# Performance work log

Measured on AMD Instinct MI355X. Metric: run time of the kernel, lower is better.

## Reference

```python
import jax, jax.numpy as jnp
import numpy as np

B, F, L, D = 256, 4, 64, 768
HID = (F + F) * 200  # 1600
NEG = -1e10


def setup_inputs() -> dict:
    key = jax.random.key(0)
    ks = jax.random.split(key, 8)
    left = jax.random.normal(ks[0], (B, F, L, D), dtype=jnp.float32)
    right = jax.random.normal(ks[1], (B, F, L, D), dtype=jnp.float32)
    # emulate ragged padding: last quarter of tokens are zero (masked out)
    left = left.at[:, :, 3 * L // 4 :, :].set(0.0)
    right = right.at[:, :, 3 * L // 4 :, :].set(0.0)
    femb_l = jax.random.normal(ks[2], (F, D), dtype=jnp.float32)
    femb_r = jax.random.normal(ks[3], (F, D), dtype=jnp.float32)
    empty_attr = jax.random.normal(ks[4], (D,), dtype=jnp.float32) * 0.05
    in_dim = 2 * F * D
    W1 = jax.random.normal(ks[5], (HID, in_dim), dtype=jnp.float32) * (1.0 / np.sqrt(in_dim))
    b1 = jnp.zeros((HID,), dtype=jnp.float32)
    W2 = jax.random.normal(ks[6], (2, HID), dtype=jnp.float32) * (1.0 / np.sqrt(HID))
    b2 = jnp.full((2,), -np.log((1 - 0.01) / 0.01), dtype=jnp.float32)
    return {"left": left, "right": right, "femb_l": femb_l, "femb_r": femb_r,
            "empty_attr": empty_attr, "W1": W1, "b1": b1, "W2": W2, "b2": b2}


def _attribute_matching(v, femb, empty_attr):
    # v: [B, F, L, D], femb: [F, D]
    tok_mask = (v != 0).sum(axis=-1) > 0          # [B, F, L]
    attr_mask = tok_mask.any(axis=-1)              # [B, F]
    logits = jnp.einsum('bfld,fd->bfl', v, femb)   # per-field attention scores
    logits = logits + jnp.where(tok_mask, 0.0, NEG)
    w = jax.nn.softmax(logits, axis=2)             # masked softmax over tokens
    summary = jnp.einsum('bfl,bfld->bfd', w, v)    # attention pooling
    return jnp.where(attr_mask[..., None], summary, empty_attr)  # [B, F, D]


def reference(left, right, femb_l, femb_r, empty_attr, W1, b1, W2, b2):
    l_rep = _attribute_matching(left, femb_l, empty_attr)
    r_rep = _attribute_matching(right, femb_r, empty_attr)
    concat = jnp.concatenate([l_rep, r_rep], axis=1).reshape(left.shape[0], -1)
    h = jax.nn.relu(concat @ W1.T + b1)
    return h @ W2.T + b2  # [B, 2]
```

## Files before the change

kernel.cpp:

```cpp
#include <hip/hip_runtime.h>

typedef __attribute__((ext_vector_type(8))) short short8;
typedef __attribute__((ext_vector_type(4))) short short4_t;
typedef __attribute__((ext_vector_type(4))) float f32x4;

#define NEGBIG -1e10f

__device__ __forceinline__ unsigned short f2bf(float x) {
  unsigned int u = __float_as_uint(x);
  u += 0x7FFFu + ((u >> 16) & 1u);
  return (unsigned short)(u >> 16);
}
__device__ __forceinline__ unsigned pack2(float a, float b) {
  unsigned ua = __float_as_uint(a), ub = __float_as_uint(b);
  ua += 0x7FFFu + ((ua >> 16) & 1u);
  ub += 0x7FFFu + ((ub >> 16) & 1u);
  return (ua >> 16) | (ub & 0xFFFF0000u);
}
__device__ __forceinline__ float lo_bf(unsigned p) { return __uint_as_float(p << 16); }
__device__ __forceinline__ float hi_bf(unsigned p) { return __uint_as_float(p & 0xFFFF0000u); }

__device__ __forceinline__ float4 mul4(float4 a, float s) {
  float4 r; r.x = a.x*s; r.y = a.y*s; r.z = a.z*s; r.w = a.w*s; return r;
}
__device__ __forceinline__ float4 add4(float4 a, float4 b) {
  float4 r; r.x = a.x+b.x; r.y = a.y+b.y; r.z = a.z+b.z; r.w = a.w+b.w; return r;
}

__global__ __launch_bounds__(512, 3) void pool_kernel(
    const float* __restrict__ left, const float* __restrict__ right,
    const float* __restrict__ femb_l, const float* __restrict__ femb_r,
    const float* __restrict__ empty_attr,
    unsigned short* __restrict__ concat)
{
  int bid  = blockIdx.x;
  int side = bid >> 10;
  int rem  = bid & 1023;
  int f    = rem & 3;
  int b    = rem >> 2;
  const float* v    = (side ? right : left) + (size_t)rem * 64 * 768;
  const float* femb = (side ? femb_r : femb_l) + f * 768;

  int tid = threadIdx.x, wave = tid >> 6, lane = tid & 63;

  const float4* fp = (const float4*)femb;
  float4 f0 = fp[lane], f1 = fp[lane + 64], f2 = fp[lane + 128];

  const float4* vp = (const float4*)(v + (size_t)wave * 8 * 768);

  float d[8];
  unsigned pk0[8], pk1[8], pk2[8], pk3[8], pk4[8], pk5[8];
  unsigned nzmask = 0;

  #pragma unroll
  for (int t = 0; t < 8; ++t) {
    float4 x0 = vp[t * 192 + lane];
    float4 x1 = vp[t * 192 + 64 + lane];
    float4 x2 = vp[t * 192 + 128 + lane];
    d[t] = x0.x*f0.x + x0.y*f0.y + x0.z*f0.z + x0.w*f0.w
         + x1.x*f1.x + x1.y*f1.y + x1.z*f1.z + x1.w*f1.w
         + x2.x*f2.x + x2.y*f2.y + x2.z*f2.z + x2.w*f2.w;
    unsigned nzb = __float_as_uint(x0.x) | __float_as_uint(x0.y)
                 | __float_as_uint(x0.z) | __float_as_uint(x0.w)
                 | __float_as_uint(x1.x) | __float_as_uint(x1.y)
                 | __float_as_uint(x1.z) | __float_as_uint(x1.w)
                 | __float_as_uint(x2.x) | __float_as_uint(x2.y)
                 | __float_as_uint(x2.z) | __float_as_uint(x2.w);
    nzmask |= (nzb != 0u) ? (1u << t) : 0u;
    pk0[t] = pack2(x0.x, x0.y); pk1[t] = pack2(x0.z, x0.w);
    pk2[t] = pack2(x1.x, x1.y); pk3[t] = pack2(x1.z, x1.w);
    pk4[t] = pack2(x2.x, x2.y); pk5[t] = pack2(x2.z, x2.w);
  }

  #pragma unroll
  for (int sh = 32; sh > 0; sh >>= 1) {
    d[0] += __shfl_xor(d[0], sh);
    d[1] += __shfl_xor(d[1], sh);
    d[2] += __shfl_xor(d[2], sh);
    d[3] += __shfl_xor(d[3], sh);
    d[4] += __shfl_xor(d[4], sh);
    d[5] += __shfl_xor(d[5], sh);
    d[6] += __shfl_xor(d[6], sh);
    d[7] += __shfl_xor(d[7], sh);
    nzmask |= __shfl_xor(nzmask, sh);
  }

  float l[8], e[8];
  #pragma unroll
  for (int t = 0; t < 8; ++t)
    l[t] = d[t] + (((nzmask >> t) & 1u) ? 0.f : NEGBIG);
  float m01 = fmaxf(l[0], l[1]), m23 = fmaxf(l[2], l[3]);
  float m45 = fmaxf(l[4], l[5]), m67 = fmaxf(l[6], l[7]);
  float m_w = fmaxf(fmaxf(m01, m23), fmaxf(m45, m67));
  #pragma unroll
  for (int t = 0; t < 8; ++t) e[t] = __expf(l[t] - m_w);
  float s_w = ((e[0]+e[1]) + (e[2]+e[3])) + ((e[4]+e[5]) + (e[6]+e[7]));

  __shared__ float m_lds[8], s_lds[8];
  __shared__ int   nz_lds[8];
  __shared__ float acc_lds[8 * 768];

  if (lane == 0) { m_lds[wave] = m_w; s_lds[wave] = s_w; nz_lds[wave] = (nzmask != 0u); }

  float4 A0 = {0,0,0,0}, A1 = {0,0,0,0}, A2 = {0,0,0,0};
  #pragma unroll
  for (int t = 0; t < 8; ++t) {
    float c = e[t];
    A0.x += c * lo_bf(pk0[t]); A0.y += c * hi_bf(pk0[t]);
    A0.z += c * lo_bf(pk1[t]); A0.w += c * hi_bf(pk1[t]);
    A1.x += c * lo_bf(pk2[t]); A1.y += c * hi_bf(pk2[t]);
    A1.z += c * lo_bf(pk3[t]); A1.w += c * hi_bf(pk3[t]);
    A2.x += c * lo_bf(pk4[t]); A2.y += c * hi_bf(pk4[t]);
    A2.z += c * lo_bf(pk5[t]); A2.w += c * hi_bf(pk5[t]);
  }

  __syncthreads();
  float M = m_lds[0];
  #pragma unroll
  for (int w = 1; w < 8; ++w) M = fmaxf(M, m_lds[w]);
  float S = 0.f;
  #pragma unroll
  for (int w = 0; w < 8; ++w) S += s_lds[w] * __expf(m_lds[w] - M);
  float scale = __expf(m_w - M) / S;

  float4* al = (float4*)acc_lds;
  al[wave * 192 +       lane] = mul4(A0, scale);
  al[wave * 192 +  64 + lane] = mul4(A1, scale);
  al[wave * 192 + 128 + lane] = mul4(A2, scale);
  __syncthreads();

  if (tid < 192) {
    float4 A = add4(add4(add4(al[tid], al[192 + tid]),
                         add4(al[384 + tid], al[576 + tid])),
                    add4(add4(al[768 + tid], al[960 + tid]),
                         add4(al[1152 + tid], al[1344 + tid])));
    int has = nz_lds[0] | nz_lds[1] | nz_lds[2] | nz_lds[3]
            | nz_lds[4] | nz_lds[5] | nz_lds[6] | nz_lds[7];
    float4 r;
    if (has) r = A;
    else     r = ((const float4*)empty_attr)[tid];
    ushort4 o;
    o.x = f2bf(r.x); o.y = f2bf(r.y); o.z = f2bf(r.z); o.w = f2bf(r.w);
    size_t base = ((size_t)b * 8 + side * 4 + f) * 192;
    ((ushort4*)concat)[base + tid] = o;
  }
}

__global__ __launch_bounds__(256) void gemm1_kernel(
    const unsigned short* __restrict__ A,
    const float* __restrict__ W1,
    float* __restrict__ Hpart)
{
  const int K = 6144, N = 1600, KC = 768;
  int colb = blockIdx.x;
  int kc   = blockIdx.y;
  int col0 = colb * 16;
  int tid = threadIdx.x, wave = tid >> 6, lane = tid & 63;

  __shared__ short wlds[96 * 16 * 8];

  const float* wsrc = W1 + (size_t)col0 * K + kc * KC;
  #pragma unroll
  for (int i = 0; i < 12; ++i) {
    int flat4 = tid + 256 * i;
    int col = flat4 / 192;
    int k   = (flat4 % 192) * 4;
    float4 w = *(const float4*)(wsrc + (size_t)col * K + k);
    short4_t o;
    o[0] = (short)f2bf(w.x); o[1] = (short)f2bf(w.y);
    o[2] = (short)f2bf(w.z); o[3] = (short)f2bf(w.w);
    *(short4_t*)(wlds + (k >> 3) * 128 + col * 8 + (k & 7)) = o;
  }
  __syncthreads();

  int lr = lane & 15;
  const short* a0 = (const short*)A + (size_t)(wave * 64 + lr) * K + kc * KC + (lane >> 4) * 8;
  const short* bptr = wlds + (lane >> 4) * 128 + lr * 8;

  f32x4 acc0 = {}, acc1 = {}, acc2 = {}, acc3 = {};

  #pragma unroll 4
  for (int ks = 0; ks < 24; ++ks) {
    short8 bf  = *(const short8*)(bptr + ks * 512);
    short8 af0 = *(const short8*)(a0 + ks * 32);
    short8 af1 = *(const short8*)(a0 + ks * 32 + 16 * K);
    short8 af2 = *(const short8*)(a0 + ks * 32 + 32 * K);
    short8 af3 = *(const short8*)(a0 + ks * 32 + 48 * K);
    acc0 = __builtin_amdgcn_mfma_f32_16x16x32_bf16(af0, bf, acc0, 0, 0, 0);
    acc1 = __builtin_amdgcn_mfma_f32_16x16x32_bf16(af1, bf, acc1, 0, 0, 0);
    acc2 = __builtin_amdgcn_mfma_f32_16x16x32_bf16(af2, bf, acc2, 0, 0, 0);
    acc3 = __builtin_amdgcn_mfma_f32_16x16x32_bf16(af3, bf, acc3, 0, 0, 0);
  }

  int ccol = lane & 15;
  int crow = (lane >> 4) * 4;
  float* hp = Hpart + (size_t)kc * 256 * N + (size_t)col0 + ccol;
  f32x4 accs[4] = {acc0, acc1, acc2, acc3};
  #pragma unroll
  for (int i = 0; i < 4; ++i) {
    int r = wave * 64 + i * 16 + crow;
    #pragma unroll
    for (int q = 0; q < 4; ++q)
      hp[(size_t)(r + q) * N] = accs[i][q];
  }
}

__global__ __launch_bounds__(256) void epilogue_kernel(
    const float* __restrict__ Hpart, const float* __restrict__ b1,
    const float* __restrict__ W2, const float* __restrict__ b2,
    float* __restrict__ out)
{
  const int N = 1600;
  int b = blockIdx.x, tid = threadIdx.x;
  int wave = tid >> 6, lane = tid & 63;
  float s0 = 0.f, s1 = 0.f;
  for (int c = tid; c < N; c += 256) {
    float acc = 0.f;
    #pragma unroll
    for (int kc = 0; kc < 8; ++kc)
      acc += Hpart[((size_t)kc * 256 + b) * N + c];
    float h = fmaxf(acc + b1[c], 0.f);
    s0 += h * W2[c];
    s1 += h * W2[N + c];
  }
  #pragma unroll
  for (int s = 32; s > 0; s >>= 1) {
    s0 += __shfl_xor(s0, s);
    s1 += __shfl_xor(s1, s);
  }
  __shared__ float r0[4], r1[4];
  if (lane == 0) { r0[wave] = s0; r1[wave] = s1; }
  __syncthreads();
  if (tid == 0) {
    out[b * 2 + 0] = r0[0] + r0[1] + r0[2] + r0[3] + b2[0];
    out[b * 2 + 1] = r1[0] + r1[1] + r1[2] + r1[3] + b2[1];
  }
}

extern "C" void kernel_launch(void* const* d_in, const int* in_sizes, int n_in,
                              void* d_out, int out_size, void* d_ws, size_t ws_size,
                              hipStream_t stream) {
  const float* left       = (const float*)d_in[0];
  const float* right      = (const float*)d_in[1];
  const float* femb_l     = (const float*)d_in[2];
  const float* femb_r     = (const float*)d_in[3];
  const float* empty_attr = (const float*)d_in[4];
  const float* W1         = (const float*)d_in[5];
  const float* b1         = (const float*)d_in[6];
  const float* W2         = (const float*)d_in[7];
  const float* b2         = (const float*)d_in[8];
  float* out = (float*)d_out;

  char* ws = (char*)d_ws;
  unsigned short* concat = (unsigned short*)ws;
  float*          Hpart  = (float*)(ws + 3145728);

  hipLaunchKernelGGL(pool_kernel, dim3(2048), dim3(512), 0, stream,
                     left, right, femb_l, femb_r, empty_attr, concat);
  hipLaunchKernelGGL(gemm1_kernel, dim3(100, 8), dim3(256), 0, stream,
                     concat, W1, Hpart);
  hipLaunchKernelGGL(epilogue_kernel, dim3(256), dim3(256), 0, stream,
                     Hpart, b1, W2, b2, out);
}
```

Before: 144.3 us.

## Split pooling into half-panel partial blocks plus a merge kernel

The single pooling kernel, which used one 512-thread block per (side,b,f) panel, is split into a partial kernel: 4096 blocks of 256 threads, each handling 32 tokens and writing an unnormalized partial sum plus (max, sum, has) metadata. A new merge kernel then combines the two halves with a log-sum-exp rescale, applies the empty-attribute fallback and writes the bf16 concat. The goal is smaller blocks and finer-grained scheduling with higher occupancy for the bandwidth-bound read of the inputs. The cost is an extra kernel launch and a write and re-read of 12 MB of fp32 partials, stored in the Hpart workspace.

```diff
diff --git a/kernel.cpp b/kernel.cpp
--- a/kernel.cpp
+++ b/kernel.cpp
@@ -27,18 +27,19 @@
   float4 r; r.x = a.x+b.x; r.y = a.y+b.y; r.z = a.z+b.z; r.w = a.w+b.w; return r;
 }
 
-__global__ __launch_bounds__(512, 3) void pool_kernel(
+__global__ __launch_bounds__(256) void pool_partial(
     const float* __restrict__ left, const float* __restrict__ right,
     const float* __restrict__ femb_l, const float* __restrict__ femb_r,
-    const float* __restrict__ empty_attr,
-    unsigned short* __restrict__ concat)
-{
-  int bid  = blockIdx.x;
-  int side = bid >> 10;
-  int rem  = bid & 1023;
-  int f    = rem & 3;
-  int b    = rem >> 2;
-  const float* v    = (side ? right : left) + (size_t)rem * 64 * 768;
+    float* __restrict__ partials,
+    float4* __restrict__ meta)
+{
+  int bid   = blockIdx.x;
+  int panel = bid >> 1;
+  int half  = bid & 1;
+  int side  = panel >> 10;
+  int rem   = panel & 1023;
+  int f     = rem & 3;
+  const float* v    = (side ? right : left) + (size_t)rem * 64 * 768 + (size_t)half * 32 * 768;
   const float* femb = (side ? femb_r : femb_l) + f * 768;
 
   int tid = threadIdx.x, wave = tid >> 6, lane = tid & 63;
@@ -96,9 +97,9 @@
   for (int t = 0; t < 8; ++t) e[t] = __expf(l[t] - m_w);
   float s_w = ((e[0]+e[1]) + (e[2]+e[3])) + ((e[4]+e[5]) + (e[6]+e[7]));
 
-  __shared__ float m_lds[8], s_lds[8];
-  __shared__ int   nz_lds[8];
-  __shared__ float acc_lds[8 * 768];
+  __shared__ float m_lds[4], s_lds[4];
+  __shared__ int   nz_lds[4];
+  __shared__ float acc_lds[4 * 768];
 
   if (lane == 0) { m_lds[wave] = m_w; s_lds[wave] = s_w; nz_lds[wave] = (nzmask != 0u); }
 
@@ -115,13 +116,10 @@
   }
 
   __syncthreads();
-  float M = m_lds[0];
-  #pragma unroll
-  for (int w = 1; w < 8; ++w) M = fmaxf(M, m_lds[w]);
-  float S = 0.f;
-  #pragma unroll
-  for (int w = 0; w < 8; ++w) S += s_lds[w] * __expf(m_lds[w] - M);
-  float scale = __expf(m_w - M) / S;
+  float M = fmaxf(fmaxf(m_lds[0], m_lds[1]), fmaxf(m_lds[2], m_lds[3]));
+  float S = s_lds[0] * __expf(m_lds[0] - M) + s_lds[1] * __expf(m_lds[1] - M)
+          + s_lds[2] * __expf(m_lds[2] - M) + s_lds[3] * __expf(m_lds[3] - M);
+  float scale = __expf(m_w - M);
 
   float4* al = (float4*)acc_lds;
   al[wave * 192 +       lane] = mul4(A0, scale);
@@ -130,20 +128,48 @@
   __syncthreads();
 
   if (tid < 192) {
-    float4 A = add4(add4(add4(al[tid], al[192 + tid]),
-                         add4(al[384 + tid], al[576 + tid])),
-                    add4(add4(al[768 + tid], al[960 + tid]),
-                         add4(al[1152 + tid], al[1344 + tid])));
-    int has = nz_lds[0] | nz_lds[1] | nz_lds[2] | nz_lds[3]
-            | nz_lds[4] | nz_lds[5] | nz_lds[6] | nz_lds[7];
-    float4 r;
-    if (has) r = A;
-    else     r = ((const float4*)empty_attr)[tid];
-    ushort4 o;
-    o.x = f2bf(r.x); o.y = f2bf(r.y); o.z = f2bf(r.z); o.w = f2bf(r.w);
-    size_t base = ((size_t)b * 8 + side * 4 + f) * 192;
-    ((ushort4*)concat)[base + tid] = o;
-  }
+    float4 A = add4(add4(al[tid], al[192 + tid]),
+                    add4(al[384 + tid], al[576 + tid]));
+    ((float4*)(partials + (size_t)bid * 768))[tid] = A;
+  }
+  if (tid == 192) {
+    int has = nz_lds[0] | nz_lds[1] | nz_lds[2] | nz_lds[3];
+    float4 mt; mt.x = M; mt.y = S; mt.z = has ? 1.f : 0.f; mt.w = 0.f;
+    meta[bid] = mt;
+  }
+}
+
+__global__ __launch_bounds__(192) void pool_merge(
+    const float* __restrict__ partials, const float4* __restrict__ meta,
+    const float* __restrict__ empty_attr,
+    unsigned short* __restrict__ concat)
+{
+  int panel = blockIdx.x;
+  int tid = threadIdx.x;
+  int side = panel >> 10;
+  int rem  = panel & 1023;
+  int f    = rem & 3;
+  int b    = rem >> 2;
+
+  float4 mt0 = meta[panel * 2], mt1 = meta[panel * 2 + 1];
+  float M = fmaxf(mt0.x, mt1.x);
+  float sc0 = __expf(mt0.x - M), sc1 = __expf(mt1.x - M);
+  float S = mt0.y * sc0 + mt1.y * sc1;
+  int has = (mt0.z != 0.f) | (mt1.z != 0.f);
+
+  float4 A0 = ((const float4*)(partials + (size_t)(panel * 2) * 768))[tid];
+  float4 A1 = ((const float4*)(partials + (size_t)(panel * 2 + 1) * 768))[tid];
+  float4 r;
+  if (has) {
+    float inv = 1.f / S;
+    r = add4(mul4(A0, sc0 * inv), mul4(A1, sc1 * inv));
+  } else {
+    r = ((const float4*)empty_attr)[tid];
+  }
+  ushort4 o;
+  o.x = f2bf(r.x); o.y = f2bf(r.y); o.z = f2bf(r.z); o.w = f2bf(r.w);
+  size_t base = ((size_t)b * 8 + side * 4 + f) * 192;
+  ((ushort4*)concat)[base + tid] = o;
 }
 
 __global__ __launch_bounds__(256) void gemm1_kernel(
@@ -254,9 +280,13 @@
   char* ws = (char*)d_ws;
   unsigned short* concat = (unsigned short*)ws;
   float*          Hpart  = (float*)(ws + 3145728);
-
-  hipLaunchKernelGGL(pool_kernel, dim3(2048), dim3(512), 0, stream,
-                     left, right, femb_l, femb_r, empty_attr, concat);
+  float*  partials = Hpart;
+  float4* meta     = (float4*)(ws + 3145728 + 12582912);
+
+  hipLaunchKernelGGL(pool_partial, dim3(4096), dim3(256), 0, stream,
+                     left, right, femb_l, femb_r, partials, meta);
+  hipLaunchKernelGGL(pool_merge, dim3(2048), dim3(192), 0, stream,
+                     partials, meta, empty_attr, concat);
   hipLaunchKernelGGL(gemm1_kernel, dim3(100, 8), dim3(256), 0, stream,
                      concat, W1, Hpart);
   hipLaunchKernelGGL(epilogue_kernel, dim3(256), dim3(256), 0, stream,
```

Measured after the change: 139.6 us. -3.3%, faster.
